# Kernel tuning notes

Measured on AMD Instinct MI355X. Metric: run time of the kernel, lower is better.

Reference implementation:

```python
import jax, jax.numpy as jnp
import numpy as np

B, S, HID = 2, 2048, 2560
HQ, HKV, HD = 8, 4, 256
WIN = 1024
EPS = 1e-6
NEG = -1e9


def _rope_tables(seq_len, head_dim, base=10000.0):
    inv = 1.0 / (base ** (jnp.arange(0, head_dim, 2, dtype=jnp.float32) / head_dim))
    t = jnp.arange(seq_len, dtype=jnp.float32)
    freqs = jnp.einsum('s,d->sd', t, inv)            # [S, HD/2]
    emb = jnp.concatenate([freqs, freqs], axis=-1)    # [S, HD]
    return jnp.cos(emb), jnp.sin(emb)


def setup_inputs() -> dict:
    key = jax.random.key(0)
    ks = jax.random.split(key, 6)
    hidden_states = jax.random.normal(ks[0], (B, S, HID), dtype=jnp.float32)
    cos1, sin1 = _rope_tables(S, HD)
    cos = jnp.broadcast_to(cos1[None], (B, S, HD)).astype(jnp.float32)
    sin = jnp.broadcast_to(sin1[None], (B, S, HD)).astype(jnp.float32)
    i = jnp.arange(S)[:, None]
    j = jnp.arange(S)[None, :]
    allowed = (j <= i) & (j > i - WIN)
    attention_mask = jnp.where(allowed, 0.0, NEG).astype(jnp.float32)
    attention_mask = jnp.broadcast_to(attention_mask[None, None], (B, 1, S, S))
    sc = 0.02
    Wq = jax.random.normal(ks[1], (HQ * HD, HID), dtype=jnp.float32) * sc
    Wk = jax.random.normal(ks[2], (HKV * HD, HID), dtype=jnp.float32) * sc
    Wv = jax.random.normal(ks[3], (HKV * HD, HID), dtype=jnp.float32) * sc
    Wo = jax.random.normal(ks[4], (HID, HQ * HD), dtype=jnp.float32) * sc
    q_norm_w = jnp.ones((HD,), dtype=jnp.float32)
    k_norm_w = jnp.ones((HD,), dtype=jnp.float32)
    return dict(hidden_states=hidden_states, cos=cos, sin=sin,
                attention_mask=attention_mask, Wq=Wq, Wk=Wk, Wv=Wv, Wo=Wo,
                q_norm_w=q_norm_w, k_norm_w=k_norm_w)


def _rms_norm(x, w=None, eps=EPS):
    x32 = x.astype(jnp.float32)
    ms = jnp.mean(x32 * x32, axis=-1, keepdims=True) + eps
    y = x32 * jax.lax.rsqrt(ms)
    if w is not None:
        y = y * w.astype(jnp.float32)
    return y.astype(x.dtype)


def _rotate_half(x):
    x1, x2 = jnp.split(x, 2, axis=-1)
    return jnp.concatenate([-x2, x1], axis=-1)


def _apply_rope(x, cos, sin):
    # x: [B,S,H,HD], cos/sin: [B,S,HD] -> unsqueeze head dim
    c = cos[:, :, None, :]
    s = sin[:, :, None, :]
    return x * c + _rotate_half(x) * s


def reference(hidden_states, cos, sin, attention_mask, Wq, Wk, Wv, Wo,
              q_norm_w, k_norm_w):
    b, s, _ = hidden_states.shape
    n_rep = HQ // HKV
    # q path: proj -> per-head RMSNorm -> RoPE -> [B,HQ,S,HD]
    q = (hidden_states @ Wq.T).reshape(b, s, HQ, HD)
    q = _rms_norm(q, q_norm_w)
    q = _apply_rope(q, cos, sin).transpose(0, 2, 1, 3)
    # k path
    k = (hidden_states @ Wk.T).reshape(b, s, HKV, HD)
    k = _rms_norm(k, k_norm_w)
    k = _apply_rope(k, cos, sin).transpose(0, 2, 1, 3)
    # v path: RMSNorm without scale, no RoPE
    v = (hidden_states @ Wv.T).reshape(b, s, HKV, HD)
    v = _rms_norm(v, None).transpose(0, 2, 1, 3)
    # GQA repeat_kv
    k = jnp.repeat(k, n_rep, axis=1)  # [B,HQ,S,HD]
    v = jnp.repeat(v, n_rep, axis=1)
    # SDPA with additive sliding-window causal mask
    scale = HD ** -0.5
    scores = jnp.einsum('bhqd,bhkd->bhqk', q, k) * scale + attention_mask
    probs = jax.nn.softmax(scores, axis=-1)
    attn = jnp.einsum('bhqk,bhkd->bhqd', probs, v)
    out = attn.transpose(0, 2, 1, 3).reshape(b, s, HQ * HD)
    return out @ Wo.T
```

## Files before the change

### kernel.cpp

```cpp
#include <hip/hip_runtime.h>

#define S_LEN 2048
#define HIDN  2560
#define HQ_N  8
#define HKV_N 4
#define HD_N  256
#define NQKV  4096
#define MROWS 4096
#define SC2   0.09016844005556021f

typedef __attribute__((ext_vector_type(8))) short bf16x8;
typedef __attribute__((ext_vector_type(4))) float f32x4;
typedef __attribute__((ext_vector_type(4))) unsigned short u16x4;
typedef __attribute__((ext_vector_type(8))) unsigned short u16x8;

typedef const __attribute__((address_space(1))) unsigned int* gas_t;
typedef __attribute__((address_space(3))) unsigned int* las_t;
#define GLDS16(gp, lp) __builtin_amdgcn_global_load_lds((gas_t)(const void*)(gp), \
                                                        (las_t)(void*)(lp), 16, 0, 0)

static __device__ __forceinline__ float bf2f(unsigned short u) {
  unsigned int x = ((unsigned int)u) << 16;
  return __builtin_bit_cast(float, x);
}
static __device__ __forceinline__ unsigned short f2bf(float f) {
  unsigned int u = __builtin_bit_cast(unsigned int, f);
  u += 0x7fffu + ((u >> 16) & 1u);
  return (unsigned short)(u >> 16);
}

__global__ void cvt_all_kernel(const float* __restrict__ hid, const float* __restrict__ Wq,
                               const float* __restrict__ Wk, const float* __restrict__ Wv,
                               const float* __restrict__ Wo, unsigned short* __restrict__ Xbf,
                               unsigned short* __restrict__ Wcat,
                               unsigned short* __restrict__ Wob) {
  int i = blockIdx.x * 256 + threadIdx.x;
  const float* src;
  unsigned short* dst;
  int j;
  if (i < 2621440) { src = hid; dst = Xbf; j = i; }
  else if (i < 3932160) { src = Wq; dst = Wcat; j = i - 2621440; }
  else if (i < 4587520) { src = Wk; dst = Wcat + 5242880; j = i - 3932160; }
  else if (i < 5242880) { src = Wv; dst = Wcat + 7864320; j = i - 4587520; }
  else { src = Wo; dst = Wob; j = i - 5242880; }
  f32x4 v = ((const f32x4*)src)[j];
  u16x4 o;
  o[0] = f2bf(v[0]); o[1] = f2bf(v[1]); o[2] = f2bf(v[2]); o[3] = f2bf(v[3]);
  ((u16x4*)dst)[j] = o;
}

template <int EPI>
__global__ __launch_bounds__(512, 2) void gemm8p(const unsigned short* __restrict__ A,
                                                 const unsigned short* __restrict__ B,
                                                 void* __restrict__ C,
                                                 int M, int N, int K, int gx,
                                                 const float* __restrict__ cosb,
                                                 const float* __restrict__ sinb,
                                                 const float* __restrict__ qw,
                                                 const float* __restrict__ kw,
                                                 unsigned short* __restrict__ qo,
                                                 unsigned short* __restrict__ ko,
                                                 unsigned short* __restrict__ vo) {
  __shared__ unsigned short ldsw[65536];
  const int tid = threadIdx.x;
  const int lane = tid & 63;
  const int w = tid >> 6;
  const int r = lane & 15, g = lane >> 4;
  const int wr = w >> 2, wc = w & 3;
  const int NT = K >> 6;

  const int nwg = gridDim.x;
  const int cpx = nwg >> 3;
  const int bid = blockIdx.x;
  const int sbid = (bid & 7) * cpx + (bid >> 3);
  const int bx = sbid % gx, by = sbid / gx;
  const int brow = by * 256, bcol = bx * 256;

  const int lr = lane >> 3;
  const int lc8 = ((lane & 7) ^ lr) * 8;
  const unsigned short* gA = A + (size_t)(brow + w * 16 + lr) * K + lc8;
  const unsigned short* gB = B + (size_t)(bcol + w * 16 + lr) * K + lc8;
  const size_t rK8 = (size_t)8 * K;
  const size_t rK128 = (size_t)128 * K;
  const int wl = w * 1024;

  const int sl0 = (((g ^ (r & 3)) + 4 * ((r >> 2) & 1))) * 8;
  int aoff[8], boff[4];
#pragma unroll
  for (int mf = 0; mf < 8; mf++) aoff[mf] = wr * 8192 + (mf * 16 + r) * 64 + sl0;
#pragma unroll
  for (int nf = 0; nf < 4; nf++)
    boff[nf] = 16384 + (wc >> 1) * 8192 + ((wc & 1) * 64 + nf * 16 + r) * 64 + sl0;

  f32x4 acc[8][4];
#pragma unroll
  for (int i = 0; i < 8; i++)
#pragma unroll
    for (int j = 0; j < 4; j++) acc[i][j] = (f32x4){0.f, 0.f, 0.f, 0.f};

  {
    unsigned short* b0 = ldsw;
    unsigned short* b1 = ldsw + 32768;
    GLDS16(gA, b0 + wl);                    GLDS16(gA + rK8, b0 + wl + 512);
    GLDS16(gA + rK128, b0 + 8192 + wl);     GLDS16(gA + rK128 + rK8, b0 + 8192 + wl + 512);
    GLDS16(gB, b0 + 16384 + wl);            GLDS16(gB + rK8, b0 + 16384 + wl + 512);
    GLDS16(gB + rK128, b0 + 24576 + wl);    GLDS16(gB + rK128 + rK8, b0 + 24576 + wl + 512);
    GLDS16(gA + 64, b1 + wl);               GLDS16(gA + 64 + rK8, b1 + wl + 512);
    GLDS16(gA + 64 + rK128, b1 + 8192 + wl); GLDS16(gA + 64 + rK128 + rK8, b1 + 8192 + wl + 512);
  }
  asm volatile("s_waitcnt vmcnt(4)" ::: "memory");
  __builtin_amdgcn_sched_barrier(0);
  __builtin_amdgcn_s_barrier();

  for (int u = 0; u < NT; ++u) {
    const unsigned short* cbp = ldsw + (u & 1) * 32768;
    unsigned short* cbw = ldsw + (u & 1) * 32768;
    unsigned short* obw = ldsw + ((u & 1) ^ 1) * 32768;
    const int c1 = (u + 1) * 64;
    const int c2 = (u + 2) * 64;
    const bool s1 = (u + 1) < NT, s2 = (u + 2) < NT;

    bf16x8 af0[4], bk0[4], af1[4];
#pragma unroll
    for (int mf = 0; mf < 4; mf++) af0[mf] = *(const bf16x8*)(cbp + aoff[mf]);
#pragma unroll
    for (int nf = 0; nf < 4; nf++) bk0[nf] = *(const bf16x8*)(cbp + boff[nf]);
#pragma unroll
    for (int mf = 0; mf < 4; mf++) af1[mf] = *(const bf16x8*)(cbp + aoff[4 + mf]);
    if (s1) {
      GLDS16(gB + c1, obw + 16384 + wl);
      GLDS16(gB + c1 + rK8, obw + 16384 + wl + 512);
    }
    __builtin_amdgcn_s_setprio(1);
#pragma unroll
    for (int mf = 0; mf < 4; mf++)
#pragma unroll
      for (int nf = 0; nf < 4; nf++)
        acc[mf][nf] = __builtin_amdgcn_mfma_f32_16x16x32_bf16(af0[mf], bk0[nf], acc[mf][nf], 0, 0, 0);
    __builtin_amdgcn_s_setprio(0);

    bf16x8 ag0[4], ag1[4];
#pragma unroll
    for (int mf = 0; mf < 4; mf++) ag0[mf] = *(const bf16x8*)(cbp + (aoff[mf] ^ 32));
#pragma unroll
    for (int mf = 0; mf < 4; mf++) ag1[mf] = *(const bf16x8*)(cbp + (aoff[4 + mf] ^ 32));
    if (s1) {
      GLDS16(gB + c1 + rK128, obw + 24576 + wl);
      GLDS16(gB + c1 + rK128 + rK8, obw + 24576 + wl + 512);
    }
    __builtin_amdgcn_s_setprio(1);
#pragma unroll
    for (int mf = 0; mf < 4; mf++)
#pragma unroll
      for (int nf = 0; nf < 4; nf++)
        acc[4 + mf][nf] = __builtin_amdgcn_mfma_f32_16x16x32_bf16(af1[mf], bk0[nf], acc[4 + mf][nf], 0, 0, 0);
    __builtin_amdgcn_s_setprio(0);
    asm volatile("s_waitcnt lgkmcnt(0)" ::: "memory");
    __builtin_amdgcn_sched_barrier(0);
    __builtin_amdgcn_s_barrier();

    bf16x8 bk1[4];
#pragma unroll
    for (int nf = 0; nf < 4; nf++) bk1[nf] = *(const bf16x8*)(cbp + (boff[nf] ^ 32));
    if (s2) {
      GLDS16(gA + c2, cbw + wl);
      GLDS16(gA + c2 + rK8, cbw + wl + 512);
    }
    __builtin_amdgcn_s_setprio(1);
#pragma unroll
    for (int mf = 0; mf < 4; mf++)
#pragma unroll
      for (int nf = 0; nf < 4; nf++)
        acc[mf][nf] = __builtin_amdgcn_mfma_f32_16x16x32_bf16(ag0[mf], bk1[nf], acc[mf][nf], 0, 0, 0);
    __builtin_amdgcn_s_setprio(0);

    if (s2) {
      GLDS16(gA + c2 + rK128, cbw + 8192 + wl);
      GLDS16(gA + c2 + rK128 + rK8, cbw + 8192 + wl + 512);
    }
    __builtin_amdgcn_s_setprio(1);
#pragma unroll
    for (int mf = 0; mf < 4; mf++)
#pragma unroll
      for (int nf = 0; nf < 4; nf++)
        acc[4 + mf][nf] = __builtin_amdgcn_mfma_f32_16x16x32_bf16(ag1[mf], bk1[nf], acc[4 + mf][nf], 0, 0, 0);
    __builtin_amdgcn_s_setprio(0);
    if (s2) { asm volatile("s_waitcnt vmcnt(4)" ::: "memory"); }
    else    { asm volatile("s_waitcnt vmcnt(0)" ::: "memory"); }
    __builtin_amdgcn_sched_barrier(0);
    __builtin_amdgcn_s_barrier();
  }

  if (EPI == 0) {
#pragma unroll
    for (int i = 0; i < 8; i++)
#pragma unroll
      for (int j = 0; j < 4; j++) {
        const int col = bcol + wc * 64 + j * 16 + r;
        const int rowb = brow + wr * 128 + i * 16 + g * 4;
#pragma unroll
        for (int e = 0; e < 4; e++)
          ((float*)C)[(size_t)(rowb + e) * N + col] = acc[i][j][e];
      }
  } else {
    const int unit = bx;
    const int bq = by >> 3;
    const int sbase = (by & 7) * 256;
    float* ldsf = (float*)ldsw;
#pragma unroll
    for (int i = 0; i < 8; i++)
#pragma unroll
      for (int e = 0; e < 4; e++) {
        float ps = 0.f;
#pragma unroll
        for (int j = 0; j < 4; j++) { float v = acc[i][j][e]; ps += v * v; }
        ps += __shfl_xor(ps, 1); ps += __shfl_xor(ps, 2);
        ps += __shfl_xor(ps, 4); ps += __shfl_xor(ps, 8);
        if (r == 0) ldsf[(wr * 128 + i * 16 + g * 4 + e) * 4 + wc] = ps;
      }
    __syncthreads();
    float inv[8][4];
#pragma unroll
    for (int i = 0; i < 8; i++)
#pragma unroll
      for (int e = 0; e < 4; e++) {
        int rl = wr * 128 + i * 16 + g * 4 + e;
        f32x4 p4 = *(const f32x4*)&ldsf[rl * 4];
        inv[i][e] = rsqrtf((p4[0] + p4[1] + p4[2] + p4[3]) * (1.0f / 256.0f) + 1e-6f);
      }
    if (unit >= 12) {
      const int hv = unit - 12;
      unsigned short* vbase = vo + (size_t)(bq * HKV_N + hv) * 64 * 8192;
      const int rsw = (r >> 1) & 3;
#pragma unroll
      for (int i = 0; i < 8; i++) {
        const int slabi = (sbase >> 5) + wr * 4 + (i >> 1);
        unsigned short* slab = vbase + (size_t)slabi * 8192;
        const int sIdx = (i & 1) * 2 + (g >> 1);
        const int soff = ((sIdx ^ rsw) << 3) + (g & 1) * 4;
#pragma unroll
        for (int j = 0; j < 4; j++) {
          const int d = wc * 64 + j * 16 + r;
          u16x4 ov;
#pragma unroll
          for (int e = 0; e < 4; e++) ov[e] = f2bf(acc[i][j][e] * inv[i][e]);
          *(u16x4*)(slab + d * 32 + soff) = ov;
        }
      }
    } else {
      const float* wvec = (unit < 8) ? qw : kw;
      const float qsc = (unit < 8) ? SC2 : 1.0f;
      float wj[4];
#pragma unroll
      for (int j = 0; j < 4; j++) wj[j] = wvec[wc * 64 + j * 16 + r] * qsc;
      __syncthreads();
#pragma unroll
      for (int i = 0; i < 8; i++)
#pragma unroll
        for (int e = 0; e < 4; e++) {
          int rl = wr * 128 + i * 16 + g * 4 + e;
          int sw = (rl & 7) << 3;
          float iv = inv[i][e];
#pragma unroll
          for (int j = 0; j < 4; j++) {
            int d = wc * 64 + j * 16 + r;
            ldsw[rl * 256 + (d ^ sw)] = f2bf(acc[i][j][e] * iv * wj[j]);
          }
        }
      __syncthreads();
      const int lr16 = lane & 15;
      const int row4 = lane >> 4;
      const int dlo = lr16 * 8, dhi = dlo + 128;
      unsigned short* qdst0 = nullptr;
      unsigned short* kbase2 = nullptr;
      if (unit < 8) qdst0 = qo + (size_t)(bq * HQ_N + unit) * S_LEN * HD_N;
      else kbase2 = ko + (size_t)(bq * HKV_N + (unit - 8)) * 64 * 8192;
#pragma unroll
      for (int it = 0; it < 8; it++) {
        const int rl2 = w * 32 + it * 4 + row4;
        const int s2 = sbase + rl2;
        const int sw2 = (rl2 & 7) << 3;
        bf16x8 ylo = *(const bf16x8*)(ldsw + rl2 * 256 + (dlo ^ sw2));
        bf16x8 yhi = *(const bf16x8*)(ldsw + rl2 * 256 + (dhi ^ sw2));
        const float* cp = cosb + (size_t)s2 * HD_N;
        const float* sp = sinb + (size_t)s2 * HD_N;
        f32x4 cA = *(const f32x4*)(cp + dlo), cB = *(const f32x4*)(cp + dlo + 4);
        f32x4 sA = *(const f32x4*)(sp + dlo), sB = *(const f32x4*)(sp + dlo + 4);
        u16x8 olo, ohi;
#pragma unroll
        for (int t = 0; t < 8; t++) {
          float a  = bf2f((unsigned short)ylo[t]);
          float b2 = bf2f((unsigned short)yhi[t]);
          float cl = (t < 4) ? cA[t] : cB[t - 4];
          float slv = (t < 4) ? sA[t] : sB[t - 4];
          olo[t] = f2bf(a * cl - b2 * slv);
          ohi[t] = f2bf(b2 * cl + a * slv);
        }
        if (unit < 8) {
          unsigned short* qd = qdst0 + (size_t)s2 * HD_N;
          *(u16x8*)(qd + dlo) = olo;
          *(u16x8*)(qd + dhi) = ohi;
        } else {
          const int kr = s2 & 31;
          unsigned short* kd = kbase2 + (size_t)(s2 >> 5) * 8192 + kr * 256;
          const int sl_ = (lr16 ^ (kr & 7)) << 3;
          *(u16x8*)(kd + sl_) = olo;
          *(u16x8*)(kd + 128 + sl_) = ohi;
        }
      }
    }
  }
}

__global__ __launch_bounds__(512) void attn_kernel(const unsigned short* __restrict__ qb,
                                                   const unsigned short* __restrict__ kb_,
                                                   const unsigned short* __restrict__ vb_,
                                                   unsigned short* __restrict__ attn) {
  __shared__ unsigned short kt[2][16384];
  __shared__ unsigned short vt[2][16384];
  const int lane = threadIdx.x & 63;
  const int w = threadIdx.x >> 6;
  const int r = lane & 15, g = lane >> 4;
  const int pblk = blockIdx.x;
  const int lb = (pblk & 7) * 32 + (pblk >> 3);
  const int qt = lb & 31;
  const int kvh = (lb >> 5) & 3;
  const int b = lb >> 7;
  const int h = kvh * 2 + (w >> 2);
  const int ww = w & 3;
  const int q0 = qt * 64;
  const int qi = q0 + ww * 16 + r;
  const int wqmin = q0 + ww * 16, wqmax = wqmin + 15;
  const unsigned short* qbase = qb + ((size_t)(b * HQ_N + h) * S_LEN + q0 + ww * 16) * HD_N;
  const unsigned short* kslabs = kb_ + (size_t)(b * HKV_N + kvh) * S_LEN * HD_N;
  const unsigned short* vslabs = vb_ + (size_t)(b * HKV_N + kvh) * S_LEN * HD_N;

  bf16x8 qf[8];
#pragma unroll
  for (int c = 0; c < 8; c++)
    qf[c] = *(const bf16x8*)(qbase + (size_t)r * HD_N + c * 32 + g * 8);

  f32x4 o[16];
#pragma unroll
  for (int i = 0; i < 16; i++) o[i] = (f32x4){0.f, 0.f, 0.f, 0.f};
  float m = -1e30f, lsum = 0.0f;

  int lo = q0 - 1023; if (lo < 0) lo = 0; lo &= ~63;
  const int hiend = q0 + 64;

  {
    const unsigned short* ks = kslabs + (size_t)(lo >> 6) * 16384;
    const unsigned short* vs = vslabs + (size_t)(lo >> 6) * 16384;
#pragma unroll
    for (int j = 0; j < 4; j++) {
      GLDS16(ks + j * 4096 + w * 512 + lane * 8, &kt[0][j * 4096 + w * 512]);
      GLDS16(vs + j * 4096 + w * 512 + lane * 8, &vt[0][j * 4096 + w * 512]);
    }
  }
  __syncthreads();

  int cur = 0;
  for (int kk = lo; kk < hiend; kk += 64) {
    if (kk + 64 < hiend) {
      const unsigned short* ks = kslabs + (size_t)((kk >> 6) + 1) * 16384;
      const unsigned short* vs = vslabs + (size_t)((kk >> 6) + 1) * 16384;
#pragma unroll
      for (int j = 0; j < 4; j++) {
        GLDS16(ks + j * 4096 + w * 512 + lane * 8, &kt[cur ^ 1][j * 4096 + w * 512]);
        GLDS16(vs + j * 4096 + w * 512 + lane * 8, &vt[cur ^ 1][j * 4096 + w * 512]);
      }
    }
#pragma unroll
    for (int s = 0; s < 2; s++) {
      const int key0 = kk + s * 32;
      if (key0 <= wqmax && key0 + 31 >= wqmin - 1023) {
        const unsigned short* kc = &kt[cur][s * 8192];
        const unsigned short* vc = &vt[cur][s * 8192];

        f32x4 st0 = (f32x4){0.f, 0.f, 0.f, 0.f}, st1 = (f32x4){0.f, 0.f, 0.f, 0.f};
        __builtin_amdgcn_s_setprio(1);
#pragma unroll
        for (int c = 0; c < 8; c++) {
          int x0 = (((c * 4 + g) ^ (r & 7)) << 3);
          bf16x8 kf0 = *(const bf16x8*)(kc + r * 256 + x0);
          bf16x8 kf1 = *(const bf16x8*)(kc + (16 + r) * 256 + x0);
          st0 = __builtin_amdgcn_mfma_f32_16x16x32_bf16(kf0, qf[c], st0, 0, 0, 0);
          st1 = __builtin_amdgcn_mfma_f32_16x16x32_bf16(kf1, qf[c], st1, 0, 0, 0);
        }
        __builtin_amdgcn_s_setprio(0);
        float p[2][4];
        float pm = -3e30f;
#pragma unroll
        for (int t = 0; t < 2; t++)
#pragma unroll
          for (int e = 0; e < 4; e++) {
            int key = key0 + t * 16 + 4 * g + e;
            float sv = (t == 0 ? st0[e] : st1[e]);
            sv = (key <= qi && key > qi - 1024) ? sv : -2e30f;
            p[t][e] = sv;
            pm = fmaxf(pm, sv);
          }
        pm = fmaxf(pm, __shfl_xor(pm, 16));
        pm = fmaxf(pm, __shfl_xor(pm, 32));
        if (!__all(pm <= m + 8.0f)) {
          float newm = fmaxf(m, pm);
          float f = exp2f(m - newm);
          m = newm;
          lsum *= f;
#pragma unroll
          for (int i = 0; i < 16; i++) {
            o[i][0] *= f; o[i][1] *= f; o[i][2] *= f; o[i][3] *= f;
          }
        }
        float ps = 0.0f;
#pragma unroll
        for (int t = 0; t < 2; t++)
#pragma unroll
          for (int e = 0; e < 4; e++) {
            float pe = exp2f(p[t][e] - m);
            p[t][e] = pe;
            ps += pe;
          }
        ps += __shfl_xor(ps, 16);
        ps += __shfl_xor(ps, 32);
        lsum += ps;
        short pk[8];
#pragma unroll
        for (int e2 = 0; e2 < 8; e2++) {
          int srcl = r + 16 * (2 * (g & 1) + (e2 >> 2));
          float a0 = __shfl(p[0][e2 & 3], srcl);
          float a1 = __shfl(p[1][e2 & 3], srcl);
          pk[e2] = (short)f2bf((g < 2) ? a0 : a1);
        }
        bf16x8 pf = {pk[0], pk[1], pk[2], pk[3], pk[4], pk[5], pk[6], pk[7]};
        int yx = ((g ^ ((r >> 1) & 3)) << 3);
        __builtin_amdgcn_s_setprio(1);
#pragma unroll
        for (int c2 = 0; c2 < 16; c2++) {
          bf16x8 vf = *(const bf16x8*)(vc + (c2 * 16 + r) * 32 + yx);
          o[c2] = __builtin_amdgcn_mfma_f32_16x16x32_bf16(vf, pf, o[c2], 0, 0, 0);
        }
        __builtin_amdgcn_s_setprio(0);
      }
    }
    __syncthreads();
    cur ^= 1;
  }
  float linv = 1.0f / lsum;
  unsigned short* arow = attn + ((size_t)(b * S_LEN) + q0 + ww * 16 + r) * (HQ_N * HD_N) + h * HD_N;
#pragma unroll
  for (int c2 = 0; c2 < 16; c2++) {
    unsigned int w0 = (unsigned)f2bf(o[c2][0] * linv) | ((unsigned)f2bf(o[c2][1] * linv) << 16);
    unsigned int w1 = (unsigned)f2bf(o[c2][2] * linv) | ((unsigned)f2bf(o[c2][3] * linv) << 16);
    *(unsigned int*)(arow + c2 * 16 + 4 * g) = w0;
    *(unsigned int*)(arow + c2 * 16 + 4 * g + 2) = w1;
  }
}

extern "C" void kernel_launch(void* const* d_in, const int* in_sizes, int n_in,
                              void* d_out, int out_size, void* d_ws, size_t ws_size,
                              hipStream_t stream) {
  const float* hid  = (const float*)d_in[0];
  const float* cosb = (const float*)d_in[1];
  const float* sinb = (const float*)d_in[2];
  const float* Wq   = (const float*)d_in[4];
  const float* Wk   = (const float*)d_in[5];
  const float* Wv   = (const float*)d_in[6];
  const float* Wo   = (const float*)d_in[7];
  const float* qw   = (const float*)d_in[8];
  const float* kw   = (const float*)d_in[9];

  char* ws = (char*)d_ws;
  unsigned short* Xbf   = (unsigned short*)(ws + 0);
  unsigned short* Wcat  = (unsigned short*)(ws + 20971520);
  unsigned short* Wob   = (unsigned short*)(ws + 41943040);
  unsigned short* qbuf  = (unsigned short*)(ws + 85983232);
  unsigned short* kbuf  = (unsigned short*)(ws + 102760448);
  unsigned short* vbuf  = (unsigned short*)(ws + 111149056);
  unsigned short* attnb = (unsigned short*)(ws + 119537664);

  cvt_all_kernel<<<25600, 256, 0, stream>>>(hid, Wq, Wk, Wv, Wo, Xbf, Wcat, Wob);
  gemm8p<1><<<256, 512, 0, stream>>>(Xbf, Wcat, nullptr, 4096, 4096, 2560, 16,
                                     cosb, sinb, qw, kw, qbuf, kbuf, vbuf);
  attn_kernel<<<256, 512, 0, stream>>>(qbuf, kbuf, vbuf, attnb);
  gemm8p<0><<<160, 512, 0, stream>>>(attnb, Wob, (float*)d_out, 4096, 2560, 2048, 10,
                                     nullptr, nullptr, nullptr, nullptr,
                                     nullptr, nullptr, nullptr);
}
```

Before: 224.2 us.

## Split QKV GEMM into dedicated 128x256-tile kernel with triple-buffered K32 pipeline

Replaces the templated 256x256-tile GEMM for the QKV projection with a dedicated kernel that uses 128x256 tiles, a K step of 32 and a three-stage LDS ring buffer. This doubles the grid from 256 to 512 blocks and shrinks LDS use so up to four blocks can be resident per CU. The aim is better CU occupancy and load balance on the 256-CU device. The cost is half the A/B reuse per tile and more barriers per unit of K. The output GEMM becomes a plain non-templated kernel with only the fp32 store epilogue.

New measurement: 236.9 us. 5.7% more time.

```diff
diff --git a/kernel.cpp b/kernel.cpp
--- a/kernel.cpp
+++ b/kernel.cpp
@@ -49,18 +49,205 @@
   ((u16x4*)dst)[j] = o;
 }
 
-template <int EPI>
-__global__ __launch_bounds__(512, 2) void gemm8p(const unsigned short* __restrict__ A,
-                                                 const unsigned short* __restrict__ B,
-                                                 void* __restrict__ C,
-                                                 int M, int N, int K, int gx,
-                                                 const float* __restrict__ cosb,
-                                                 const float* __restrict__ sinb,
-                                                 const float* __restrict__ qw,
-                                                 const float* __restrict__ kw,
-                                                 unsigned short* __restrict__ qo,
-                                                 unsigned short* __restrict__ ko,
-                                                 unsigned short* __restrict__ vo) {
+__global__ __launch_bounds__(512, 4) void gemmqkv(const unsigned short* __restrict__ A,
+                                                  const unsigned short* __restrict__ B,
+                                                  int K,
+                                                  const float* __restrict__ cosb,
+                                                  const float* __restrict__ sinb,
+                                                  const float* __restrict__ qw,
+                                                  const float* __restrict__ kw,
+                                                  unsigned short* __restrict__ qo,
+                                                  unsigned short* __restrict__ ko,
+                                                  unsigned short* __restrict__ vo) {
+  __shared__ unsigned short lds3[36864];
+  const int tid = threadIdx.x;
+  const int lane = tid & 63;
+  const int w = tid >> 6;
+  const int r = lane & 15, g = lane >> 4;
+  const int wr = w >> 2, wc = w & 3;
+  const int NT = K >> 5;
+
+  const int bid = blockIdx.x;
+  const int sbid = (bid & 7) * 64 + (bid >> 3);
+  const int bx = sbid & 15, by = sbid >> 4;
+  const int brow = by * 128;
+
+  const int srow = w * 16 + (lane >> 2);
+  const int sw8 = ((lane & 3) ^ ((lane >> 3) & 3)) * 8;
+  const unsigned short* gA = A + (size_t)(brow + srow) * K + sw8;
+  const unsigned short* gB0 = B + (size_t)(bx * 256 + srow) * K + sw8;
+  const unsigned short* gB1 = B + (size_t)(bx * 256 + 128 + srow) * K + sw8;
+  const int wl = w * 512;
+
+  const int sl0 = (g ^ ((r >> 1) & 3)) * 8;
+  int aoff[4], boff[4];
+#pragma unroll
+  for (int mf = 0; mf < 4; mf++) aoff[mf] = (wr * 64 + mf * 16 + r) * 32 + sl0;
+#pragma unroll
+  for (int nf = 0; nf < 4; nf++) boff[nf] = 4096 + (wc * 64 + nf * 16 + r) * 32 + sl0;
+
+  f32x4 acc[4][4];
+#pragma unroll
+  for (int i = 0; i < 4; i++)
+#pragma unroll
+    for (int j = 0; j < 4; j++) acc[i][j] = (f32x4){0.f, 0.f, 0.f, 0.f};
+
+  {
+    unsigned short* b0 = lds3;
+    unsigned short* b1 = lds3 + 12288;
+    GLDS16(gA, b0 + wl); GLDS16(gB0, b0 + 4096 + wl); GLDS16(gB1, b0 + 8192 + wl);
+    GLDS16(gA + 32, b1 + wl); GLDS16(gB0 + 32, b1 + 4096 + wl); GLDS16(gB1 + 32, b1 + 8192 + wl);
+  }
+  asm volatile("s_waitcnt vmcnt(3)" ::: "memory");
+  __builtin_amdgcn_sched_barrier(0);
+  __builtin_amdgcn_s_barrier();
+
+  int o_c = 0, o_n = 12288, o_s = 24576;
+  for (int t = 0; t < NT; ++t) {
+    const unsigned short* cb = lds3 + o_c;
+    unsigned short* sb = lds3 + o_s;
+    const int kc2 = (t + 2) << 5;
+    const bool st = (t + 2) < NT;
+
+    bf16x8 af[4], bf[4];
+#pragma unroll
+    for (int mf = 0; mf < 4; mf++) af[mf] = *(const bf16x8*)(cb + aoff[mf]);
+#pragma unroll
+    for (int nf = 0; nf < 4; nf++) bf[nf] = *(const bf16x8*)(cb + boff[nf]);
+    if (st) {
+      GLDS16(gA + kc2, sb + wl);
+      GLDS16(gB0 + kc2, sb + 4096 + wl);
+      GLDS16(gB1 + kc2, sb + 8192 + wl);
+    }
+    asm volatile("s_waitcnt lgkmcnt(0)" ::: "memory");
+    __builtin_amdgcn_sched_barrier(0);
+    __builtin_amdgcn_s_setprio(1);
+#pragma unroll
+    for (int mf = 0; mf < 4; mf++)
+#pragma unroll
+      for (int nf = 0; nf < 4; nf++)
+        acc[mf][nf] = __builtin_amdgcn_mfma_f32_16x16x32_bf16(af[mf], bf[nf], acc[mf][nf], 0, 0, 0);
+    __builtin_amdgcn_s_setprio(0);
+    if (st) { asm volatile("s_waitcnt vmcnt(3)" ::: "memory"); }
+    else    { asm volatile("s_waitcnt vmcnt(0)" ::: "memory"); }
+    __builtin_amdgcn_sched_barrier(0);
+    __builtin_amdgcn_s_barrier();
+
+    int tmp = o_c; o_c = o_n; o_n = o_s; o_s = tmp;
+  }
+
+  const int unit = bx;
+  const int bq = by >> 4;
+  const int sbase = (by & 15) * 128;
+  float* ldsf = (float*)lds3;
+#pragma unroll
+  for (int i = 0; i < 4; i++)
+#pragma unroll
+    for (int e = 0; e < 4; e++) {
+      float ps = 0.f;
+#pragma unroll
+      for (int j = 0; j < 4; j++) { float v = acc[i][j][e]; ps += v * v; }
+      ps += __shfl_xor(ps, 1); ps += __shfl_xor(ps, 2);
+      ps += __shfl_xor(ps, 4); ps += __shfl_xor(ps, 8);
+      if (r == 0) ldsf[(wr * 64 + i * 16 + g * 4 + e) * 4 + wc] = ps;
+    }
+  __syncthreads();
+  float inv[4][4];
+#pragma unroll
+  for (int i = 0; i < 4; i++)
+#pragma unroll
+    for (int e = 0; e < 4; e++) {
+      int rl = wr * 64 + i * 16 + g * 4 + e;
+      f32x4 p4 = *(const f32x4*)&ldsf[rl * 4];
+      inv[i][e] = rsqrtf((p4[0] + p4[1] + p4[2] + p4[3]) * (1.0f / 256.0f) + 1e-6f);
+    }
+  if (unit >= 12) {
+    const int hv = unit - 12;
+    unsigned short* vbase = vo + (size_t)(bq * HKV_N + hv) * 64 * 8192;
+    const int rsw = (r >> 1) & 3;
+#pragma unroll
+    for (int i = 0; i < 4; i++) {
+      const int slabi = (sbase >> 5) + wr * 2 + (i >> 1);
+      unsigned short* slab = vbase + (size_t)slabi * 8192;
+      const int sIdx = (i & 1) * 2 + (g >> 1);
+      const int soff = ((sIdx ^ rsw) << 3) + (g & 1) * 4;
+#pragma unroll
+      for (int j = 0; j < 4; j++) {
+        const int d = wc * 64 + j * 16 + r;
+        u16x4 ov;
+#pragma unroll
+        for (int e = 0; e < 4; e++) ov[e] = f2bf(acc[i][j][e] * inv[i][e]);
+        *(u16x4*)(slab + d * 32 + soff) = ov;
+      }
+    }
+  } else {
+    const float* wvec = (unit < 8) ? qw : kw;
+    const float qsc = (unit < 8) ? SC2 : 1.0f;
+    float wj[4];
+#pragma unroll
+    for (int j = 0; j < 4; j++) wj[j] = wvec[wc * 64 + j * 16 + r] * qsc;
+    __syncthreads();
+#pragma unroll
+    for (int i = 0; i < 4; i++)
+#pragma unroll
+      for (int e = 0; e < 4; e++) {
+        int rl = wr * 64 + i * 16 + g * 4 + e;
+        int sw = (rl & 7) << 3;
+        float iv = inv[i][e];
+#pragma unroll
+        for (int j = 0; j < 4; j++) {
+          int d = wc * 64 + j * 16 + r;
+          lds3[rl * 256 + (d ^ sw)] = f2bf(acc[i][j][e] * iv * wj[j]);
+        }
+      }
+    __syncthreads();
+    const int lr16 = lane & 15;
+    const int row4 = lane >> 4;
+    const int dlo = lr16 * 8, dhi = dlo + 128;
+    unsigned short* qdst0 = nullptr;
+    unsigned short* kbase2 = nullptr;
+    if (unit < 8) qdst0 = qo + (size_t)(bq * HQ_N + unit) * S_LEN * HD_N;
+    else kbase2 = ko + (size_t)(bq * HKV_N + (unit - 8)) * 64 * 8192;
+#pragma unroll
+    for (int it = 0; it < 4; it++) {
+      const int rl2 = w * 16 + it * 4 + row4;
+      const int s2 = sbase + rl2;
+      const int sw2 = (rl2 & 7) << 3;
+      bf16x8 ylo = *(const bf16x8*)(lds3 + rl2 * 256 + (dlo ^ sw2));
+      bf16x8 yhi = *(const bf16x8*)(lds3 + rl2 * 256 + (dhi ^ sw2));
+      const float* cp = cosb + (size_t)s2 * HD_N;
+      const float* sp = sinb + (size_t)s2 * HD_N;
+      f32x4 cA = *(const f32x4*)(cp + dlo), cB = *(const f32x4*)(cp + dlo + 4);
+      f32x4 sA = *(const f32x4*)(sp + dlo), sB = *(const f32x4*)(sp + dlo + 4);
+      u16x8 olo, ohi;
+#pragma unroll
+      for (int tt = 0; tt < 8; tt++) {
+        float a  = bf2f((unsigned short)ylo[tt]);
+        float b2 = bf2f((unsigned short)yhi[tt]);
+        float cl = (tt < 4) ? cA[tt] : cB[tt - 4];
+        float slv = (tt < 4) ? sA[tt] : sB[tt - 4];
+        olo[tt] = f2bf(a * cl - b2 * slv);
+        ohi[tt] = f2bf(b2 * cl + a * slv);
+      }
+      if (unit < 8) {
+        unsigned short* qd = qdst0 + (size_t)s2 * HD_N;
+        *(u16x8*)(qd + dlo) = olo;
+        *(u16x8*)(qd + dhi) = ohi;
+      } else {
+        const int kr = s2 & 31;
+        unsigned short* kd = kbase2 + (size_t)(s2 >> 5) * 8192 + kr * 256;
+        const int sl_ = (lr16 ^ (kr & 7)) << 3;
+        *(u16x8*)(kd + sl_) = olo;
+        *(u16x8*)(kd + 128 + sl_) = ohi;
+      }
+    }
+  }
+}
+
+__global__ __launch_bounds__(512, 2) void gemm_out(const unsigned short* __restrict__ A,
+                                                   const unsigned short* __restrict__ B,
+                                                   float* __restrict__ C,
+                                                   int M, int N, int K, int gx) {
   __shared__ unsigned short ldsw[65536];
   const int tid = threadIdx.x;
   const int lane = tid & 63;
@@ -191,125 +378,16 @@
     __builtin_amdgcn_s_barrier();
   }
 
-  if (EPI == 0) {
-#pragma unroll
-    for (int i = 0; i < 8; i++)
-#pragma unroll
-      for (int j = 0; j < 4; j++) {
-        const int col = bcol + wc * 64 + j * 16 + r;
-        const int rowb = brow + wr * 128 + i * 16 + g * 4;
-#pragma unroll
-        for (int e = 0; e < 4; e++)
-          ((float*)C)[(size_t)(rowb + e) * N + col] = acc[i][j][e];
-      }
-  } else {
-    const int unit = bx;
-    const int bq = by >> 3;
-    const int sbase = (by & 7) * 256;
-    float* ldsf = (float*)ldsw;
-#pragma unroll
-    for (int i = 0; i < 8; i++)
-#pragma unroll
-      for (int e = 0; e < 4; e++) {
-        float ps = 0.f;
-#pragma unroll
-        for (int j = 0; j < 4; j++) { float v = acc[i][j][e]; ps += v * v; }
-        ps += __shfl_xor(ps, 1); ps += __shfl_xor(ps, 2);
-        ps += __shfl_xor(ps, 4); ps += __shfl_xor(ps, 8);
-        if (r == 0) ldsf[(wr * 128 + i * 16 + g * 4 + e) * 4 + wc] = ps;
-      }
-    __syncthreads();
-    float inv[8][4];
-#pragma unroll
-    for (int i = 0; i < 8; i++)
-#pragma unroll
-      for (int e = 0; e < 4; e++) {
-        int rl = wr * 128 + i * 16 + g * 4 + e;
-        f32x4 p4 = *(const f32x4*)&ldsf[rl * 4];
-        inv[i][e] = rsqrtf((p4[0] + p4[1] + p4[2] + p4[3]) * (1.0f / 256.0f) + 1e-6f);
-      }
-    if (unit >= 12) {
-      const int hv = unit - 12;
-      unsigned short* vbase = vo + (size_t)(bq * HKV_N + hv) * 64 * 8192;
-      const int rsw = (r >> 1) & 3;
-#pragma unroll
-      for (int i = 0; i < 8; i++) {
-        const int slabi = (sbase >> 5) + wr * 4 + (i >> 1);
-        unsigned short* slab = vbase + (size_t)slabi * 8192;
-        const int sIdx = (i & 1) * 2 + (g >> 1);
-        const int soff = ((sIdx ^ rsw) << 3) + (g & 1) * 4;
-#pragma unroll
-        for (int j = 0; j < 4; j++) {
-          const int d = wc * 64 + j * 16 + r;
-          u16x4 ov;
-#pragma unroll
-          for (int e = 0; e < 4; e++) ov[e] = f2bf(acc[i][j][e] * inv[i][e]);
-          *(u16x4*)(slab + d * 32 + soff) = ov;
-        }
-      }
-    } else {
-      const float* wvec = (unit < 8) ? qw : kw;
-      const float qsc = (unit < 8) ? SC2 : 1.0f;
-      float wj[4];
-#pragma unroll
-      for (int j = 0; j < 4; j++) wj[j] = wvec[wc * 64 + j * 16 + r] * qsc;
-      __syncthreads();
-#pragma unroll
-      for (int i = 0; i < 8; i++)
-#pragma unroll
-        for (int e = 0; e < 4; e++) {
-          int rl = wr * 128 + i * 16 + g * 4 + e;
-          int sw = (rl & 7) << 3;
-          float iv = inv[i][e];
-#pragma unroll
-          for (int j = 0; j < 4; j++) {
-            int d = wc * 64 + j * 16 + r;
-            ldsw[rl * 256 + (d ^ sw)] = f2bf(acc[i][j][e] * iv * wj[j]);
-          }
-        }
-      __syncthreads();
-      const int lr16 = lane & 15;
-      const int row4 = lane >> 4;
-      const int dlo = lr16 * 8, dhi = dlo + 128;
-      unsigned short* qdst0 = nullptr;
-      unsigned short* kbase2 = nullptr;
-      if (unit < 8) qdst0 = qo + (size_t)(bq * HQ_N + unit) * S_LEN * HD_N;
-      else kbase2 = ko + (size_t)(bq * HKV_N + (unit - 8)) * 64 * 8192;
-#pragma unroll
-      for (int it = 0; it < 8; it++) {
-        const int rl2 = w * 32 + it * 4 + row4;
-        const int s2 = sbase + rl2;
-        const int sw2 = (rl2 & 7) << 3;
-        bf16x8 ylo = *(const bf16x8*)(ldsw + rl2 * 256 + (dlo ^ sw2));
-        bf16x8 yhi = *(const bf16x8*)(ldsw + rl2 * 256 + (dhi ^ sw2));
-        const float* cp = cosb + (size_t)s2 * HD_N;
-        const float* sp = sinb + (size_t)s2 * HD_N;
-        f32x4 cA = *(const f32x4*)(cp + dlo), cB = *(const f32x4*)(cp + dlo + 4);
-        f32x4 sA = *(const f32x4*)(sp + dlo), sB = *(const f32x4*)(sp + dlo + 4);
-        u16x8 olo, ohi;
-#pragma unroll
-        for (int t = 0; t < 8; t++) {
-          float a  = bf2f((unsigned short)ylo[t]);
-          float b2 = bf2f((unsigned short)yhi[t]);
-          float cl = (t < 4) ? cA[t] : cB[t - 4];
-          float slv = (t < 4) ? sA[t] : sB[t - 4];
-          olo[t] = f2bf(a * cl - b2 * slv);
-          ohi[t] = f2bf(b2 * cl + a * slv);
-        }
-        if (unit < 8) {
-          unsigned short* qd = qdst0 + (size_t)s2 * HD_N;
-          *(u16x8*)(qd + dlo) = olo;
-          *(u16x8*)(qd + dhi) = ohi;
-        } else {
-          const int kr = s2 & 31;
-          unsigned short* kd = kbase2 + (size_t)(s2 >> 5) * 8192 + kr * 256;
-          const int sl_ = (lr16 ^ (kr & 7)) << 3;
-          *(u16x8*)(kd + sl_) = olo;
-          *(u16x8*)(kd + 128 + sl_) = ohi;
-        }
-      }
-    }
-  }
+#pragma unroll
+  for (int i = 0; i < 8; i++)
+#pragma unroll
+    for (int j = 0; j < 4; j++) {
+      const int col = bcol + wc * 64 + j * 16 + r;
+      const int rowb = brow + wr * 128 + i * 16 + g * 4;
+#pragma unroll
+      for (int e = 0; e < 4; e++)
+        C[(size_t)(rowb + e) * N + col] = acc[i][j][e];
+    }
 }
 
 __global__ __launch_bounds__(512) void attn_kernel(const unsigned short* __restrict__ qb,
@@ -480,10 +558,7 @@
   unsigned short* attnb = (unsigned short*)(ws + 119537664);
 
   cvt_all_kernel<<<25600, 256, 0, stream>>>(hid, Wq, Wk, Wv, Wo, Xbf, Wcat, Wob);
-  gemm8p<1><<<256, 512, 0, stream>>>(Xbf, Wcat, nullptr, 4096, 4096, 2560, 16,
-                                     cosb, sinb, qw, kw, qbuf, kbuf, vbuf);
+  gemmqkv<<<512, 512, 0, stream>>>(Xbf, Wcat, 2560, cosb, sinb, qw, kw, qbuf, kbuf, vbuf);
   attn_kernel<<<256, 512, 0, stream>>>(qbuf, kbuf, vbuf, attnb);
-  gemm8p<0><<<160, 512, 0, stream>>>(attnb, Wob, (float*)d_out, 4096, 2560, 2048, 10,
-                                     nullptr, nullptr, nullptr, nullptr,
-                                     nullptr, nullptr, nullptr);
-}
+  gemm_out<<<160, 512, 0, stream>>>(attnb, Wob, (float*)d_out, 4096, 2560, 2048, 10);
+}
```

## Apply RoPE in registers by remapping B-tile columns, dropping LDS staging

Applied to the files above, without the earlier changes.

For the fused QKV GEMM epilogue (EPI != 0), the B-tile column assignment is remapped so each lane holds both the d and d+128 halves of a head dimension. RoPE can then be applied directly from accumulator registers, which removes the LDS round-trip and the two __syncthreads. The cost is that stores become scalar 2-byte writes to global memory, and cos/sin reads become scalar strided loads. Both are less coalesced than the previous 16-byte vector accesses.

Result: slower. 238.2 us (+6.2%).

```diff
diff --git a/kernel.cpp b/kernel.cpp
--- a/kernel.cpp
+++ b/kernel.cpp
@@ -12,7 +12,6 @@
 typedef __attribute__((ext_vector_type(8))) short bf16x8;
 typedef __attribute__((ext_vector_type(4))) float f32x4;
 typedef __attribute__((ext_vector_type(4))) unsigned short u16x4;
-typedef __attribute__((ext_vector_type(8))) unsigned short u16x8;
 
 typedef const __attribute__((address_space(1))) unsigned int* gas_t;
 typedef __attribute__((address_space(3))) unsigned int* las_t;
@@ -89,8 +88,12 @@
 #pragma unroll
   for (int mf = 0; mf < 8; mf++) aoff[mf] = wr * 8192 + (mf * 16 + r) * 64 + sl0;
 #pragma unroll
-  for (int nf = 0; nf < 4; nf++)
-    boff[nf] = 16384 + (wc >> 1) * 8192 + ((wc & 1) * 64 + nf * 16 + r) * 64 + sl0;
+  for (int nf = 0; nf < 4; nf++) {
+    if (EPI == 0)
+      boff[nf] = 16384 + (wc >> 1) * 8192 + ((wc & 1) * 64 + nf * 16 + r) * 64 + sl0;
+    else
+      boff[nf] = 16384 + (nf >> 1) * 8192 + (wc * 32 + (nf & 1) * 16 + r) * 64 + sl0;
+  }
 
   f32x4 acc[8][4];
 #pragma unroll
@@ -239,11 +242,11 @@
         const int sIdx = (i & 1) * 2 + (g >> 1);
         const int soff = ((sIdx ^ rsw) << 3) + (g & 1) * 4;
 #pragma unroll
-        for (int j = 0; j < 4; j++) {
-          const int d = wc * 64 + j * 16 + r;
+        for (int nf = 0; nf < 4; nf++) {
+          const int d = (nf >> 1) * 128 + wc * 32 + (nf & 1) * 16 + r;
           u16x4 ov;
 #pragma unroll
-          for (int e = 0; e < 4; e++) ov[e] = f2bf(acc[i][j][e] * inv[i][e]);
+          for (int e = 0; e < 4; e++) ov[e] = f2bf(acc[i][nf][e] * inv[i][e]);
           *(u16x4*)(slab + d * 32 + soff) = ov;
         }
       }
@@ -252,62 +255,50 @@
       const float qsc = (unit < 8) ? SC2 : 1.0f;
       float wj[4];
 #pragma unroll
-      for (int j = 0; j < 4; j++) wj[j] = wvec[wc * 64 + j * 16 + r] * qsc;
-      __syncthreads();
-#pragma unroll
-      for (int i = 0; i < 8; i++)
-#pragma unroll
-        for (int e = 0; e < 4; e++) {
-          int rl = wr * 128 + i * 16 + g * 4 + e;
-          int sw = (rl & 7) << 3;
-          float iv = inv[i][e];
-#pragma unroll
-          for (int j = 0; j < 4; j++) {
-            int d = wc * 64 + j * 16 + r;
-            ldsw[rl * 256 + (d ^ sw)] = f2bf(acc[i][j][e] * iv * wj[j]);
-          }
-        }
-      __syncthreads();
-      const int lr16 = lane & 15;
-      const int row4 = lane >> 4;
-      const int dlo = lr16 * 8, dhi = dlo + 128;
+      for (int nf = 0; nf < 4; nf++) {
+        const int d = (nf >> 1) * 128 + wc * 32 + (nf & 1) * 16 + r;
+        wj[nf] = wvec[d] * qsc;
+      }
       unsigned short* qdst0 = nullptr;
       unsigned short* kbase2 = nullptr;
       if (unit < 8) qdst0 = qo + (size_t)(bq * HQ_N + unit) * S_LEN * HD_N;
       else kbase2 = ko + (size_t)(bq * HKV_N + (unit - 8)) * 64 * 8192;
 #pragma unroll
-      for (int it = 0; it < 8; it++) {
-        const int rl2 = w * 32 + it * 4 + row4;
-        const int s2 = sbase + rl2;
-        const int sw2 = (rl2 & 7) << 3;
-        bf16x8 ylo = *(const bf16x8*)(ldsw + rl2 * 256 + (dlo ^ sw2));
-        bf16x8 yhi = *(const bf16x8*)(ldsw + rl2 * 256 + (dhi ^ sw2));
-        const float* cp = cosb + (size_t)s2 * HD_N;
-        const float* sp = sinb + (size_t)s2 * HD_N;
-        f32x4 cA = *(const f32x4*)(cp + dlo), cB = *(const f32x4*)(cp + dlo + 4);
-        f32x4 sA = *(const f32x4*)(sp + dlo), sB = *(const f32x4*)(sp + dlo + 4);
-        u16x8 olo, ohi;
-#pragma unroll
-        for (int t = 0; t < 8; t++) {
-          float a  = bf2f((unsigned short)ylo[t]);
-          float b2 = bf2f((unsigned short)yhi[t]);
-          float cl = (t < 4) ? cA[t] : cB[t - 4];
-          float slv = (t < 4) ? sA[t] : sB[t - 4];
-          olo[t] = f2bf(a * cl - b2 * slv);
-          ohi[t] = f2bf(b2 * cl + a * slv);
-        }
-        if (unit < 8) {
-          unsigned short* qd = qdst0 + (size_t)s2 * HD_N;
-          *(u16x8*)(qd + dlo) = olo;
-          *(u16x8*)(qd + dhi) = ohi;
-        } else {
-          const int kr = s2 & 31;
-          unsigned short* kd = kbase2 + (size_t)(s2 >> 5) * 8192 + kr * 256;
-          const int sl_ = (lr16 ^ (kr & 7)) << 3;
-          *(u16x8*)(kd + sl_) = olo;
-          *(u16x8*)(kd + 128 + sl_) = ohi;
-        }
-      }
+      for (int i = 0; i < 8; i++)
+#pragma unroll
+        for (int e = 0; e < 4; e++) {
+          const int rl = wr * 128 + i * 16 + g * 4 + e;
+          const int s2r = sbase + rl;
+          const float iv = inv[i][e];
+          const float* cp = cosb + (size_t)s2r * HD_N;
+          const float* sp = sinb + (size_t)s2r * HD_N;
+          unsigned short* qd = nullptr;
+          unsigned short* kd = nullptr;
+          int kr = 0;
+          if (unit < 8) qd = qdst0 + (size_t)s2r * HD_N;
+          else {
+            kr = s2r & 31;
+            kd = kbase2 + (size_t)(s2r >> 5) * 8192 + kr * 256;
+          }
+#pragma unroll
+          for (int p = 0; p < 2; p++) {
+            const int dlo = wc * 32 + p * 16 + r;
+            const float cv = cp[dlo];
+            const float sn = sp[dlo];
+            const float ylo = acc[i][p][e] * iv * wj[p];
+            const float yhi = acc[i][p + 2][e] * iv * wj[p + 2];
+            const unsigned short olo = f2bf(ylo * cv - yhi * sn);
+            const unsigned short ohi = f2bf(yhi * cv + ylo * sn);
+            if (unit < 8) {
+              qd[dlo] = olo;
+              qd[dlo + 128] = ohi;
+            } else {
+              const int klo = (((dlo >> 3) ^ (kr & 7)) << 3) + (dlo & 7);
+              kd[klo] = olo;
+              kd[klo + 128] = ohi;
+            }
+          }
+        }
     }
   }
 }
```
